# Kernel tuning notes

Hardware: AMD Instinct MI355X
Metric: run time of the kernel (lower is better)

## Reference

```python
import jax, jax.numpy as jnp
import numpy as np

LOG_DT_MIN, LOG_DT_MAX = np.log(0.001), np.log(0.1)


def setup_inputs() -> dict:
    L, H, P = 8192, 512, 256
    key = jax.random.key(0)
    ks = jax.random.split(key, 8)
    # continuous-time diagonal state matrix: Re < 0 for stability (HiPPO-like)
    Lambda_re = -(0.1 + jax.random.uniform(ks[0], (P,), dtype=jnp.float32))
    Lambda_im = jnp.pi * jax.random.normal(ks[1], (P,), dtype=jnp.float32)
    # B ~ Vinv @ B_init stored as (...,2) real/imag; C ~ C_init @ V likewise
    B = jax.random.normal(ks[2], (P, H, 2), dtype=jnp.float32) / np.sqrt(2.0 * P)
    C = jax.random.normal(ks[3], (H, P, 2), dtype=jnp.float32) / np.sqrt(2.0 * P)
    D = jax.random.normal(ks[4], (H,), dtype=jnp.float32)
    log_step = (jax.random.uniform(ks[5], (P,), dtype=jnp.float32)
                * (LOG_DT_MAX - LOG_DT_MIN) + LOG_DT_MIN)
    input_sequence = jax.random.normal(ks[6], (L, H), dtype=jnp.float32)
    hidden = jnp.zeros((1, P), dtype=jnp.float32)  # initial state (real part; imag 0)
    resets = jax.random.randint(ks[7], (L,), 0, 2, dtype=jnp.int32)
    return dict(hidden=hidden, input_sequence=input_sequence, Lambda_re=Lambda_re,
                Lambda_im=Lambda_im, B=B, C=C, D=D, log_step=log_step, resets=resets)


def _binary_operator_reset(q_i, q_j):
    A_i, b_i, c_i = q_i
    A_j, b_j, c_j = q_j
    return (A_j * A_i * (1 - c_j) + A_j * c_j,
            (A_j * b_i + b_j) * (1 - c_j) + b_j * c_j,
            c_i * (1 - c_j) + c_j)


def reference(hidden, input_sequence, Lambda_re, Lambda_im, B, C, D, log_step, resets):
    # S5SSM forward: zoh discretization, conj_sym=True, step_rescale=1.0
    Lambda = (Lambda_re + 1j * Lambda_im).astype(jnp.complex64)           # (P,)
    B_tilde = (B[..., 0] + 1j * B[..., 1]).astype(jnp.complex64)          # (P,H)
    C_tilde = (C[..., 0] + 1j * C[..., 1]).astype(jnp.complex64)          # (H,P)
    step = jnp.exp(log_step)                                              # (P,)
    # zero-order-hold discretization
    Lambda_bar = jnp.exp(Lambda * step)                                   # (P,)
    B_bar = ((Lambda_bar - 1.0) / Lambda)[:, None] * B_tilde              # (P,H)

    L, P = input_sequence.shape[0], Lambda.shape[0]
    Bu = input_sequence.astype(jnp.complex64) @ B_bar.T                   # (L,P)
    Lambda_elems = jnp.concatenate(
        [jnp.ones((1, P), Lambda_bar.dtype), jnp.broadcast_to(Lambda_bar, (L, P))])
    Bu_elems = jnp.concatenate([hidden.astype(jnp.complex64), Bu])        # (L+1,P)
    r = jnp.concatenate([jnp.zeros((1,), jnp.float32),
                         resets.astype(jnp.float32)])[:, None]            # (L+1,1)

    _, xs, _ = jax.lax.associative_scan(_binary_operator_reset,
                                        (Lambda_elems, Bu_elems, r))
    xs = xs[1:]                                                           # (L,P)
    ys = 2.0 * (xs @ C_tilde.T).real                                      # conj_sym factor 2, (L,H)
    out = ys + input_sequence * D                                         # feedthrough Du
    return out
```

## Files before the change

### kernel.cpp

```cpp
#include <hip/hip_runtime.h>

#define L_LEN 8192
#define H_DIM 512
#define P_DIM 256
#define N2P   512
#define CHUNKS 512
#define CLEN  (L_LEN / CHUNKS)

typedef short bf16x8 __attribute__((ext_vector_type(8)));
typedef float f32x4  __attribute__((ext_vector_type(4)));

#define OFF_BMT   0
#define OFF_W2T   (OFF_BMT + 131072)
#define OFF_LBRE  (OFF_W2T + 131072)
#define OFF_LBIM  (OFF_LBRE + 256)
#define OFF_BU    (OFF_LBIM + 256)
#define OFF_XC    (OFF_BU + L_LEN * 512)
#define OFF_AGAR  (OFF_XC + L_LEN * 256)
#define OFF_AGAI  (OFF_AGAR + CHUNKS * P_DIM)
#define OFF_AGBR  (OFF_AGAI + CHUNKS * P_DIM)
#define OFF_AGBI  (OFF_AGBR + CHUNKS * P_DIM)
#define OFF_AGC   (OFF_AGBI + CHUNKS * P_DIM)
#define OFF_CARR  (OFF_AGC  + CHUNKS)
#define OFF_CARI  (OFF_CARR + CHUNKS * P_DIM)

__device__ __forceinline__ unsigned short bfr(float x) {
    unsigned u = __float_as_uint(x);
    u = (u + 0x7fffu + ((u >> 16) & 1u)) >> 16;
    return (unsigned short)u;
}
__device__ __forceinline__ unsigned pk(float a, float b) {
    return (unsigned)bfr(a) | ((unsigned)bfr(b) << 16);
}

__global__ __launch_bounds__(256) void s5_k0(
    const float* __restrict__ Lre, const float* __restrict__ Lim,
    const float* __restrict__ logstep,
    const float* __restrict__ B,
    const float* __restrict__ C,
    short* __restrict__ BmT, unsigned* __restrict__ W2Tu,
    float* __restrict__ Lbre, float* __restrict__ Lbim)
{
    int idx = blockIdx.x * 256 + threadIdx.x;

    int p = idx >> 9, h = idx & 511;
    float lre = Lre[p], lim = Lim[p];
    float s = expf(logstep[p]);
    float er = expf(lre * s);
    float lbr = er * cosf(lim * s);
    float lbi = er * sinf(lim * s);
    if (h == 0) { Lbre[p] = lbr; Lbim[p] = lbi; }
    float nr = lbr - 1.0f, ni = lbi;
    float inv = 1.0f / (lre * lre + lim * lim);
    float fr = (nr * lre + ni * lim) * inv;
    float fi = (ni * lre - nr * lim) * inv;
    float b0 = B[2 * idx + 0];
    float b1 = B[2 * idx + 1];
    BmT[(size_t)p * 512 + h]         = (short)bfr(fr * b0 - fi * b1);
    BmT[(size_t)(256 + p) * 512 + h] = (short)bfr(fr * b1 + fi * b0);

    int hh = idx >> 8, pp = idx & 255;
    float cre = C[2 * idx + 0];
    float cim = C[2 * idx + 1];
    W2Tu[(size_t)hh * 256 + pp] = pk(2.0f * cre, -2.0f * cim);
}

template<bool AFP32, bool EPI>
__global__ __launch_bounds__(256) void s5_gemm(
    const void* __restrict__ Ap, const short* __restrict__ WT,
    const float* __restrict__ u, const float* __restrict__ Dv,
    float* __restrict__ Out)
{
    __shared__ __align__(16) short lds[2][2][64][72];

    const int tid = threadIdx.x;
    const int rowBase = blockIdx.y * 64;
    const int colBase = blockIdx.x * 64;
    const int srow = tid >> 2;
    const int scq  = (tid & 3) * 16;

    const int w = tid >> 6, l = tid & 63;
    const int wr = (w >> 1) * 32, wc = (w & 1) * 32;
    const int fr = l & 15, fq = l >> 4;

    int4 ra0, ra1, rb0, rb1;

    auto LOAD = [&](int t) {
        const int kk = t * 64;
        if (AFP32) {
            const float* A = (const float*)Ap;
            const float4* sa = (const float4*)(A + (size_t)(rowBase + srow) * 512 + kk + scq);
            float4 f0 = sa[0], f1 = sa[1], f2 = sa[2], f3 = sa[3];
            ra0 = make_int4((int)pk(f0.x,f0.y), (int)pk(f0.z,f0.w), (int)pk(f1.x,f1.y), (int)pk(f1.z,f1.w));
            ra1 = make_int4((int)pk(f2.x,f2.y), (int)pk(f2.z,f2.w), (int)pk(f3.x,f3.y), (int)pk(f3.z,f3.w));
        } else {
            const short* A = (const short*)Ap;
            const int4* sa = (const int4*)(A + (size_t)(rowBase + srow) * 512 + kk + scq);
            ra0 = sa[0]; ra1 = sa[1];
        }
        const int4* sb = (const int4*)(WT + (size_t)(colBase + srow) * 512 + kk + scq);
        rb0 = sb[0]; rb1 = sb[1];
    };
    auto WRITE = [&](int buf) {
        *(int4*)&lds[buf][0][srow][scq]     = ra0;
        *(int4*)&lds[buf][0][srow][scq + 8] = ra1;
        *(int4*)&lds[buf][1][srow][scq]     = rb0;
        *(int4*)&lds[buf][1][srow][scq + 8] = rb1;
    };

    f32x4 acc[2][2] = {};

    auto COMPUTE = [&](int buf) {
        #pragma unroll
        for (int kc = 0; kc < 2; ++kc) {
            bf16x8 a0 = *(const bf16x8*)&lds[buf][0][wr +      fr][kc * 32 + 8 * fq];
            bf16x8 a1 = *(const bf16x8*)&lds[buf][0][wr + 16 + fr][kc * 32 + 8 * fq];
            bf16x8 b0 = *(const bf16x8*)&lds[buf][1][wc +      fr][kc * 32 + 8 * fq];
            bf16x8 b1 = *(const bf16x8*)&lds[buf][1][wc + 16 + fr][kc * 32 + 8 * fq];
            acc[0][0] = __builtin_amdgcn_mfma_f32_16x16x32_bf16(a0, b0, acc[0][0], 0, 0, 0);
            acc[0][1] = __builtin_amdgcn_mfma_f32_16x16x32_bf16(a0, b1, acc[0][1], 0, 0, 0);
            acc[1][0] = __builtin_amdgcn_mfma_f32_16x16x32_bf16(a1, b0, acc[1][0], 0, 0, 0);
            acc[1][1] = __builtin_amdgcn_mfma_f32_16x16x32_bf16(a1, b1, acc[1][1], 0, 0, 0);
        }
    };

    LOAD(0); WRITE(0); __syncthreads();
    #pragma unroll
    for (int t = 0; t < 8; ++t) {
        if (t + 1 < 8) LOAD(t + 1);
        COMPUTE(t & 1);
        if (t + 1 < 8) WRITE((t + 1) & 1);
        __syncthreads();
    }

    float dv0 = 0.f, dv1 = 0.f;
    if (EPI) { dv0 = Dv[colBase + wc + fr]; dv1 = Dv[colBase + wc + 16 + fr]; }

    #pragma unroll
    for (int i = 0; i < 2; ++i)
        #pragma unroll
        for (int j = 0; j < 2; ++j)
            #pragma unroll
            for (int q = 0; q < 4; ++q) {
                int r = rowBase + wr + 16 * i + fq * 4 + q;
                int c = colBase + wc + 16 * j + fr;
                float v = acc[i][j][q];
                if (EPI) v += u[(size_t)r * 512 + c] * (j ? dv1 : dv0);
                Out[(size_t)r * 512 + c] = v;
            }
}

__global__ __launch_bounds__(P_DIM) void s5_k2(
    const float* __restrict__ Bu, const int* __restrict__ resets,
    const float* __restrict__ Lbre, const float* __restrict__ Lbim,
    float* __restrict__ aAr, float* __restrict__ aAi,
    float* __restrict__ aBr, float* __restrict__ aBi, float* __restrict__ aC)
{
    const int p = threadIdx.x, ci = blockIdx.x;
    const float lbr = Lbre[p], lbi = Lbim[p];
    float Ar = 1.f, Ai = 0.f, br = 0.f, bi = 0.f;
    int c = 0;
    const int t0 = ci * CLEN;
    for (int t = t0; t < t0 + CLEN; ++t) {
        int rs = resets[t];
        float bur = Bu[(size_t)t * 512 + p];
        float bui = Bu[(size_t)t * 512 + 256 + p];
        if (rs) { Ar = lbr; Ai = lbi; br = bur; bi = bui; c = 1; }
        else {
            float nAr = lbr * Ar - lbi * Ai; Ai = lbr * Ai + lbi * Ar; Ar = nAr;
            float nbr = lbr * br - lbi * bi + bur; bi = lbr * bi + lbi * br + bui; br = nbr;
        }
    }
    aAr[ci * P_DIM + p] = Ar; aAi[ci * P_DIM + p] = Ai;
    aBr[ci * P_DIM + p] = br; aBi[ci * P_DIM + p] = bi;
    if (p == 0) aC[ci] = (float)c;
}

__global__ __launch_bounds__(CHUNKS) void s5_k3p(
    const float* __restrict__ hidden,
    const float* __restrict__ aAr, const float* __restrict__ aAi,
    const float* __restrict__ aBr, const float* __restrict__ aBi,
    const float* __restrict__ aC,
    float* __restrict__ carR, float* __restrict__ carI)
{
    __shared__ float sAr[CHUNKS], sAi[CHUNKS], sBr[CHUNKS], sBi[CHUNKS], sC[CHUNKS];
    const int p = blockIdx.x, t = threadIdx.x;

    float Ar = aAr[t * P_DIM + p], Ai = aAi[t * P_DIM + p];
    float br = aBr[t * P_DIM + p], bi = aBi[t * P_DIM + p];
    float c  = aC[t];
    sAr[t] = Ar; sAi[t] = Ai; sBr[t] = br; sBi[t] = bi; sC[t] = c;
    __syncthreads();

    for (int s = 1; s < CHUNKS; s <<= 1) {
        float pAr = 0.f, pAi = 0.f, pBr = 0.f, pBi = 0.f, pC = 0.f;
        const bool has = (t >= s);
        if (has) { pAr = sAr[t-s]; pAi = sAi[t-s]; pBr = sBr[t-s]; pBi = sBi[t-s]; pC = sC[t-s]; }
        __syncthreads();
        if (has) {
            if (c <= 0.5f) {
                float nAr = Ar * pAr - Ai * pAi;
                float nAi = Ar * pAi + Ai * pAr;
                float nbr = Ar * pBr - Ai * pBi + br;
                float nbi = Ar * pBi + Ai * pBr + bi;
                Ar = nAr; Ai = nAi; br = nbr; bi = nbi; c = pC;
            }
            sAr[t] = Ar; sAi[t] = Ai; sBr[t] = br; sBi[t] = bi; sC[t] = c;
        }
        __syncthreads();
    }

    const float h = hidden[p];
    float sr, si;
    if (t == 0) { sr = h; si = 0.f; }
    else {
        float gAr = sAr[t-1], gAi = sAi[t-1], gBr = sBr[t-1], gBi = sBi[t-1], gC = sC[t-1];
        if (gC > 0.5f) { sr = gBr; si = gBi; }
        else           { sr = gAr * h + gBr; si = gAi * h + gBi; }
    }
    carR[t * P_DIM + p] = sr;
    carI[t * P_DIM + p] = si;
}

__global__ __launch_bounds__(P_DIM) void s5_k4(
    const float* __restrict__ Bu, const int* __restrict__ resets,
    const float* __restrict__ Lbre, const float* __restrict__ Lbim,
    const float* __restrict__ carR, const float* __restrict__ carI,
    unsigned* __restrict__ xcu)
{
    const int p = threadIdx.x, ci = blockIdx.x;
    const float lbr = Lbre[p], lbi = Lbim[p];
    float sr = carR[ci * P_DIM + p];
    float si = carI[ci * P_DIM + p];
    const int t0 = ci * CLEN;
    for (int t = t0; t < t0 + CLEN; ++t) {
        int rs = resets[t];
        float bur = Bu[(size_t)t * 512 + p];
        float bui = Bu[(size_t)t * 512 + 256 + p];
        if (rs) { sr = bur; si = bui; }
        else {
            float nr = lbr * sr - lbi * si + bur;
            si = lbr * si + lbi * sr + bui;
            sr = nr;
        }
        xcu[(size_t)t * 256 + p] = pk(sr, si);
    }
}

extern "C" void kernel_launch(void* const* d_in, const int* in_sizes, int n_in,
                              void* d_out, int out_size, void* d_ws, size_t ws_size,
                              hipStream_t stream)
{
    const float* hidden  = (const float*)d_in[0];
    const float* u       = (const float*)d_in[1];
    const float* Lre     = (const float*)d_in[2];
    const float* Lim     = (const float*)d_in[3];
    const float* B       = (const float*)d_in[4];
    const float* C       = (const float*)d_in[5];
    const float* D       = (const float*)d_in[6];
    const float* logstep = (const float*)d_in[7];
    const int*   resets  = (const int*)d_in[8];
    float* out = (float*)d_out;
    float* ws  = (float*)d_ws;

    short*    BmT  = (short*)(ws + OFF_BMT);
    short*    W2T  = (short*)(ws + OFF_W2T);
    unsigned* W2Tu = (unsigned*)(ws + OFF_W2T);
    float*    Lbre = ws + OFF_LBRE;
    float*    Lbim = ws + OFF_LBIM;
    float*    Bu   = ws + OFF_BU;
    short*    xc   = (short*)(ws + OFF_XC);
    unsigned* xcu  = (unsigned*)(ws + OFF_XC);

    s5_k0<<<512, 256, 0, stream>>>(Lre, Lim, logstep, B, C, BmT, W2Tu, Lbre, Lbim);

    s5_gemm<true, false><<<dim3(N2P / 64, L_LEN / 64), 256, 0, stream>>>(
        (const void*)u, BmT, nullptr, nullptr, Bu);

    s5_k2<<<CHUNKS, P_DIM, 0, stream>>>(Bu, resets, Lbre, Lbim,
        ws + OFF_AGAR, ws + OFF_AGAI, ws + OFF_AGBR, ws + OFF_AGBI, ws + OFF_AGC);

    s5_k3p<<<P_DIM, CHUNKS, 0, stream>>>(hidden,
        ws + OFF_AGAR, ws + OFF_AGAI, ws + OFF_AGBR, ws + OFF_AGBI, ws + OFF_AGC,
        ws + OFF_CARR, ws + OFF_CARI);

    s5_k4<<<CHUNKS, P_DIM, 0, stream>>>(Bu, resets, Lbre, Lbim,
        ws + OFF_CARR, ws + OFF_CARI, xcu);

    s5_gemm<false, true><<<dim3(H_DIM / 64, L_LEN / 64), 256, 0, stream>>>(
        (const void*)xc, W2T, u, D, out);
}
```

Measured before the change: 68.99 us.

## Store Bu in bf16, enlarge GEMM tiles, stage operands via direct global-to-LDS loads

The intermediate Bu is now written as bf16 instead of fp32, halving its write traffic in the first GEMM and its read traffic in both scan passes. The GEMM tile grows from 64x64 to 128x64 with 8 accumulators per wave. bf16 operands are staged with global_load_lds, bypassing registers, and the unpadded LDS layout drops the previous row padding. This risks LDS bank conflicts and adds bf16 rounding error to Bu before the recurrence.

```diff
diff --git a/kernel.cpp b/kernel.cpp
--- a/kernel.cpp
+++ b/kernel.cpp
@@ -15,8 +15,8 @@
 #define OFF_LBRE  (OFF_W2T + 131072)
 #define OFF_LBIM  (OFF_LBRE + 256)
 #define OFF_BU    (OFF_LBIM + 256)
-#define OFF_XC    (OFF_BU + L_LEN * 512)
-#define OFF_AGAR  (OFF_XC + L_LEN * 256)
+#define OFF_XC    (OFF_BU + 2097152)
+#define OFF_AGAR  (OFF_XC + 2097152)
 #define OFF_AGAI  (OFF_AGAR + CHUNKS * P_DIM)
 #define OFF_AGBR  (OFF_AGAI + CHUNKS * P_DIM)
 #define OFF_AGBI  (OFF_AGBR + CHUNKS * P_DIM)
@@ -31,6 +31,14 @@
 }
 __device__ __forceinline__ unsigned pk(float a, float b) {
     return (unsigned)bfr(a) | ((unsigned)bfr(b) << 16);
+}
+__device__ __forceinline__ float b2f(unsigned short v) {
+    return __uint_as_float(((unsigned)v) << 16);
+}
+__device__ __forceinline__ void gl2lds16(const void* g, void* l) {
+    __builtin_amdgcn_global_load_lds(
+        (const __attribute__((address_space(1))) void*)g,
+        (__attribute__((address_space(3))) void*)l, 16, 0, 0);
 }
 
 __global__ __launch_bounds__(256) void s5_k0(
@@ -69,89 +77,130 @@
 __global__ __launch_bounds__(256) void s5_gemm(
     const void* __restrict__ Ap, const short* __restrict__ WT,
     const float* __restrict__ u, const float* __restrict__ Dv,
-    float* __restrict__ Out)
-{
-    __shared__ __align__(16) short lds[2][2][64][72];
+    void* __restrict__ Outp)
+{
+    __shared__ __align__(16) short sA[2][128][64];
+    __shared__ __align__(16) short sB[2][64][64];
 
     const int tid = threadIdx.x;
-    const int rowBase = blockIdx.y * 64;
+    const int rowBase = blockIdx.y * 128;
     const int colBase = blockIdx.x * 64;
-    const int srow = tid >> 2;
-    const int scq  = (tid & 3) * 16;
 
     const int w = tid >> 6, l = tid & 63;
-    const int wr = (w >> 1) * 32, wc = (w & 1) * 32;
+    const int wr = (w >> 1) * 64, wc = (w & 1) * 32;
     const int fr = l & 15, fq = l >> 4;
 
-    int4 ra0, ra1, rb0, rb1;
-
-    auto LOAD = [&](int t) {
+    float4 fa[8];
+    f32x4 acc[4][2] = {};
+
+    auto STAGE_B = [&](int bf, int t) {
         const int kk = t * 64;
-        if (AFP32) {
-            const float* A = (const float*)Ap;
-            const float4* sa = (const float4*)(A + (size_t)(rowBase + srow) * 512 + kk + scq);
-            float4 f0 = sa[0], f1 = sa[1], f2 = sa[2], f3 = sa[3];
-            ra0 = make_int4((int)pk(f0.x,f0.y), (int)pk(f0.z,f0.w), (int)pk(f1.x,f1.y), (int)pk(f1.z,f1.w));
-            ra1 = make_int4((int)pk(f2.x,f2.y), (int)pk(f2.z,f2.w), (int)pk(f3.x,f3.y), (int)pk(f3.z,f3.w));
-        } else {
-            const short* A = (const short*)Ap;
-            const int4* sa = (const int4*)(A + (size_t)(rowBase + srow) * 512 + kk + scq);
-            ra0 = sa[0]; ra1 = sa[1];
-        }
-        const int4* sb = (const int4*)(WT + (size_t)(colBase + srow) * 512 + kk + scq);
-        rb0 = sb[0]; rb1 = sb[1];
-    };
-    auto WRITE = [&](int buf) {
-        *(int4*)&lds[buf][0][srow][scq]     = ra0;
-        *(int4*)&lds[buf][0][srow][scq + 8] = ra1;
-        *(int4*)&lds[buf][1][srow][scq]     = rb0;
-        *(int4*)&lds[buf][1][srow][scq + 8] = rb1;
-    };
-
-    f32x4 acc[2][2] = {};
-
-    auto COMPUTE = [&](int buf) {
+        #pragma unroll
+        for (int i = 0; i < 2; ++i) {
+            int e = i * 256 + tid;
+            int row = e >> 3, c8 = (e & 7) << 3;
+            gl2lds16(WT + (size_t)(colBase + row) * 512 + kk + c8, &sB[bf][row][c8]);
+        }
+    };
+    auto STAGE_A16 = [&](int bf, int t) {
+        const int kk = t * 64;
+        const short* A = (const short*)Ap;
+        #pragma unroll
+        for (int i = 0; i < 4; ++i) {
+            int e = i * 256 + tid;
+            int row = e >> 3, c8 = (e & 7) << 3;
+            gl2lds16(A + (size_t)(rowBase + row) * 512 + kk + c8, &sA[bf][row][c8]);
+        }
+    };
+    auto LOADA_REG = [&](int t) {
+        const int kk = t * 64;
+        const float* A = (const float*)Ap;
+        #pragma unroll
+        for (int i = 0; i < 4; ++i) {
+            int e = i * 256 + tid;
+            int row = e >> 3, c8 = (e & 7) << 3;
+            const float4* s = (const float4*)(A + (size_t)(rowBase + row) * 512 + kk + c8);
+            fa[2 * i] = s[0]; fa[2 * i + 1] = s[1];
+        }
+    };
+    auto CONVA_WRITE = [&](int bf) {
+        #pragma unroll
+        for (int i = 0; i < 4; ++i) {
+            int e = i * 256 + tid;
+            int row = e >> 3, c8 = (e & 7) << 3;
+            float4 f0 = fa[2 * i], f1 = fa[2 * i + 1];
+            int4 wv = make_int4((int)pk(f0.x, f0.y), (int)pk(f0.z, f0.w),
+                                (int)pk(f1.x, f1.y), (int)pk(f1.z, f1.w));
+            *(int4*)&sA[bf][row][c8] = wv;
+        }
+    };
+    auto COMPUTE = [&](int bf) {
         #pragma unroll
         for (int kc = 0; kc < 2; ++kc) {
-            bf16x8 a0 = *(const bf16x8*)&lds[buf][0][wr +      fr][kc * 32 + 8 * fq];
-            bf16x8 a1 = *(const bf16x8*)&lds[buf][0][wr + 16 + fr][kc * 32 + 8 * fq];
-            bf16x8 b0 = *(const bf16x8*)&lds[buf][1][wc +      fr][kc * 32 + 8 * fq];
-            bf16x8 b1 = *(const bf16x8*)&lds[buf][1][wc + 16 + fr][kc * 32 + 8 * fq];
-            acc[0][0] = __builtin_amdgcn_mfma_f32_16x16x32_bf16(a0, b0, acc[0][0], 0, 0, 0);
-            acc[0][1] = __builtin_amdgcn_mfma_f32_16x16x32_bf16(a0, b1, acc[0][1], 0, 0, 0);
-            acc[1][0] = __builtin_amdgcn_mfma_f32_16x16x32_bf16(a1, b0, acc[1][0], 0, 0, 0);
-            acc[1][1] = __builtin_amdgcn_mfma_f32_16x16x32_bf16(a1, b1, acc[1][1], 0, 0, 0);
-        }
-    };
-
-    LOAD(0); WRITE(0); __syncthreads();
-    #pragma unroll
+            bf16x8 av[4], bv[2];
+            #pragma unroll
+            for (int i = 0; i < 4; ++i)
+                av[i] = *(const bf16x8*)&sA[bf][wr + 16 * i + fr][kc * 32 + 8 * fq];
+            #pragma unroll
+            for (int j = 0; j < 2; ++j)
+                bv[j] = *(const bf16x8*)&sB[bf][wc + 16 * j + fr][kc * 32 + 8 * fq];
+            #pragma unroll
+            for (int i = 0; i < 4; ++i)
+                #pragma unroll
+                for (int j = 0; j < 2; ++j)
+                    acc[i][j] = __builtin_amdgcn_mfma_f32_16x16x32_bf16(av[i], bv[j], acc[i][j], 0, 0, 0);
+        }
+    };
+
+    if (AFP32) { LOADA_REG(0); CONVA_WRITE(0); } else { STAGE_A16(0, 0); }
+    STAGE_B(0, 0);
+    __syncthreads();
+
     for (int t = 0; t < 8; ++t) {
-        if (t + 1 < 8) LOAD(t + 1);
-        COMPUTE(t & 1);
-        if (t + 1 < 8) WRITE((t + 1) & 1);
+        const int cur = t & 1, nxt = cur ^ 1;
+        if (t < 7) {
+            STAGE_B(nxt, t + 1);
+            if (AFP32) LOADA_REG(t + 1); else STAGE_A16(nxt, t + 1);
+        }
+        COMPUTE(cur);
+        if (AFP32 && t < 7) CONVA_WRITE(nxt);
         __syncthreads();
     }
 
-    float dv0 = 0.f, dv1 = 0.f;
-    if (EPI) { dv0 = Dv[colBase + wc + fr]; dv1 = Dv[colBase + wc + 16 + fr]; }
-
-    #pragma unroll
-    for (int i = 0; i < 2; ++i)
-        #pragma unroll
-        for (int j = 0; j < 2; ++j)
-            #pragma unroll
-            for (int q = 0; q < 4; ++q) {
-                int r = rowBase + wr + 16 * i + fq * 4 + q;
-                int c = colBase + wc + 16 * j + fr;
-                float v = acc[i][j][q];
-                if (EPI) v += u[(size_t)r * 512 + c] * (j ? dv1 : dv0);
-                Out[(size_t)r * 512 + c] = v;
-            }
+    if (AFP32) {
+        unsigned short* Out = (unsigned short*)Outp;
+        #pragma unroll
+        for (int i = 0; i < 4; ++i)
+            #pragma unroll
+            for (int j = 0; j < 2; ++j)
+                #pragma unroll
+                for (int q = 0; q < 4; ++q) {
+                    int r = rowBase + wr + 16 * i + fq * 4 + q;
+                    int c = colBase + wc + 16 * j + fr;
+                    Out[(size_t)r * 512 + c] = bfr(acc[i][j][q]);
+                }
+    } else {
+        float* Out = (float*)Outp;
+        float dj[2];
+        #pragma unroll
+        for (int j = 0; j < 2; ++j) dj[j] = EPI ? Dv[colBase + wc + 16 * j + fr] : 0.f;
+        #pragma unroll
+        for (int i = 0; i < 4; ++i)
+            #pragma unroll
+            for (int j = 0; j < 2; ++j)
+                #pragma unroll
+                for (int q = 0; q < 4; ++q) {
+                    int r = rowBase + wr + 16 * i + fq * 4 + q;
+                    int c = colBase + wc + 16 * j + fr;
+                    float v = acc[i][j][q];
+                    if (EPI) v += u[(size_t)r * 512 + c] * dj[j];
+                    Out[(size_t)r * 512 + c] = v;
+                }
+    }
 }
 
 __global__ __launch_bounds__(P_DIM) void s5_k2(
-    const float* __restrict__ Bu, const int* __restrict__ resets,
+    const unsigned short* __restrict__ Bu, const int* __restrict__ resets,
     const float* __restrict__ Lbre, const float* __restrict__ Lbim,
     float* __restrict__ aAr, float* __restrict__ aAi,
     float* __restrict__ aBr, float* __restrict__ aBi, float* __restrict__ aC)
@@ -163,8 +212,8 @@
     const int t0 = ci * CLEN;
     for (int t = t0; t < t0 + CLEN; ++t) {
         int rs = resets[t];
-        float bur = Bu[(size_t)t * 512 + p];
-        float bui = Bu[(size_t)t * 512 + 256 + p];
+        float bur = b2f(Bu[(size_t)t * 512 + p]);
+        float bui = b2f(Bu[(size_t)t * 512 + 256 + p]);
         if (rs) { Ar = lbr; Ai = lbi; br = bur; bi = bui; c = 1; }
         else {
             float nAr = lbr * Ar - lbi * Ai; Ai = lbr * Ai + lbi * Ar; Ar = nAr;
@@ -223,7 +272,7 @@
 }
 
 __global__ __launch_bounds__(P_DIM) void s5_k4(
-    const float* __restrict__ Bu, const int* __restrict__ resets,
+    const unsigned short* __restrict__ Bu, const int* __restrict__ resets,
     const float* __restrict__ Lbre, const float* __restrict__ Lbim,
     const float* __restrict__ carR, const float* __restrict__ carI,
     unsigned* __restrict__ xcu)
@@ -235,8 +284,8 @@
     const int t0 = ci * CLEN;
     for (int t = t0; t < t0 + CLEN; ++t) {
         int rs = resets[t];
-        float bur = Bu[(size_t)t * 512 + p];
-        float bui = Bu[(size_t)t * 512 + 256 + p];
+        float bur = b2f(Bu[(size_t)t * 512 + p]);
+        float bui = b2f(Bu[(size_t)t * 512 + 256 + p]);
         if (rs) { sr = bur; si = bui; }
         else {
             float nr = lbr * sr - lbi * si + bur;
@@ -263,19 +312,19 @@
     float* out = (float*)d_out;
     float* ws  = (float*)d_ws;
 
-    short*    BmT  = (short*)(ws + OFF_BMT);
-    short*    W2T  = (short*)(ws + OFF_W2T);
-    unsigned* W2Tu = (unsigned*)(ws + OFF_W2T);
-    float*    Lbre = ws + OFF_LBRE;
-    float*    Lbim = ws + OFF_LBIM;
-    float*    Bu   = ws + OFF_BU;
-    short*    xc   = (short*)(ws + OFF_XC);
-    unsigned* xcu  = (unsigned*)(ws + OFF_XC);
+    short*          BmT  = (short*)(ws + OFF_BMT);
+    short*          W2T  = (short*)(ws + OFF_W2T);
+    unsigned*       W2Tu = (unsigned*)(ws + OFF_W2T);
+    float*          Lbre = ws + OFF_LBRE;
+    float*          Lbim = ws + OFF_LBIM;
+    unsigned short* Bu   = (unsigned short*)(ws + OFF_BU);
+    short*          xc   = (short*)(ws + OFF_XC);
+    unsigned*       xcu  = (unsigned*)(ws + OFF_XC);
 
     s5_k0<<<512, 256, 0, stream>>>(Lre, Lim, logstep, B, C, BmT, W2Tu, Lbre, Lbim);
 
-    s5_gemm<true, false><<<dim3(N2P / 64, L_LEN / 64), 256, 0, stream>>>(
-        (const void*)u, BmT, nullptr, nullptr, Bu);
+    s5_gemm<true, false><<<dim3(N2P / 64, L_LEN / 128), 256, 0, stream>>>(
+        (const void*)u, BmT, nullptr, nullptr, (void*)Bu);
 
     s5_k2<<<CHUNKS, P_DIM, 0, stream>>>(Bu, resets, Lbre, Lbim,
         ws + OFF_AGAR, ws + OFF_AGAI, ws + OFF_AGBR, ws + OFF_AGBI, ws + OFF_AGC);
@@ -287,6 +336,6 @@
     s5_k4<<<CHUNKS, P_DIM, 0, stream>>>(Bu, resets, Lbre, Lbim,
         ws + OFF_CARR, ws + OFF_CARI, xcu);
 
-    s5_gemm<false, true><<<dim3(H_DIM / 64, L_LEN / 64), 256, 0, stream>>>(
-        (const void*)xc, W2T, u, D, out);
-}
+    s5_gemm<false, true><<<dim3(H_DIM / 64, L_LEN / 128), 256, 0, stream>>>(
+        (const void*)xc, W2T, u, D, (void*)out);
+}
```

After: 70.23 us. No clear change (+1.8%).
